# Kernel optimization log

Hardware: AMD Instinct MI355X
Metric: run time of the kernel (lower is better)

The kernel has to match this reference:

```python
import jax, jax.numpy as jnp
import numpy as np

N = 500_000      # total rows (e.g. video frames)
S = 10_000       # number of segments (shots)
D_IN = 128
D_OUT = 128


def setup_inputs() -> dict:
    key = jax.random.key(0)
    k1, k2, k3 = jax.random.split(key, 3)
    inp = jax.random.normal(k1, (N, D_IN), dtype=jnp.float32)
    # contiguous non-overlapping segments covering [0, N): graph[j] = (start_j, end_j) inclusive
    rng = np.random.default_rng(0)
    cuts = np.sort(rng.choice(np.arange(1, N), size=S - 1, replace=False))
    starts = np.concatenate([[0], cuts]).astype(np.int64)
    ends = np.concatenate([cuts - 1, [N - 1]]).astype(np.int64)
    graph = jnp.asarray(np.stack([starts, ends], axis=1))  # [S, 2]
    # nn.Linear params (kaiming-uniform-ish scale is irrelevant for correctness baseline)
    W = jax.random.normal(k2, (D_OUT, D_IN), dtype=jnp.float32) * (1.0 / np.sqrt(D_IN))
    b = jax.random.normal(k3, (D_OUT,), dtype=jnp.float32) * 0.01
    return {"input": inp, "graph": graph, "W": W, "b": b}


def reference(input, graph, W, b):
    # One big GEMM for the projection (instead of per-segment Linear calls) ...
    y = input @ W.T + b                              # [N, D_OUT]
    n = input.shape[0]
    s = graph.shape[0]
    starts = graph[:, 0]
    ends = graph[:, 1]
    rows = jnp.arange(n)
    # ... then a single irregular segment reduction over ragged boundaries.
    seg_id = jnp.clip(jnp.searchsorted(starts, rows, side="right") - 1, 0, s - 1)  # [N]
    valid = (rows >= starts[seg_id]) & (rows <= ends[seg_id])  # guards any uncovered rows
    y = jnp.where(valid[:, None], y, 0.0)
    return jax.ops.segment_sum(y, seg_id, num_segments=s)     # [S, D_OUT]
```

## Files before the change

### kernel.cpp

```cpp
#include <hip/hip_runtime.h>
#include <hip/hip_bf16.h>


#define D 128
#define D4 32

__device__ __forceinline__ void f4add(float4& a, const float4& v) {
  a.x += v.x; a.y += v.y; a.z += v.z; a.w += v.w;
}

__global__ __launch_bounds__(256) void seg_sum_kernel(
    const float* __restrict__ in, const int* __restrict__ graph,
    float* __restrict__ Xs, int N, int S) {
  int s   = blockIdx.x;
  int tid = threadIdx.x;
  int rg  = tid >> 5;
  int c4  = tid & 31;

  int rs  = graph[2 * s];
  int re  = graph[2 * s + 1];
  int nxt = (s + 1 < S) ? (graph[2 * s + 2] - 1) : (N - 1);
  re = min(re, min(nxt, N - 1));
  rs = max(rs, 0);
  int cnt = max(0, re - rs + 1);

  const float4* p = (const float4*)in + (size_t)rs * D4 + c4;
  float4 a0 = make_float4(0.f, 0.f, 0.f, 0.f);
  float4 a1 = make_float4(0.f, 0.f, 0.f, 0.f);

  int r = rg;
  for (; r + 8 < cnt; r += 16) {
    float4 v0 = p[r * D4];
    float4 v1 = p[(r + 8) * D4];
    f4add(a0, v0);
    f4add(a1, v1);
  }
  for (; r < cnt; r += 8) {
    float4 v0 = p[r * D4];
    f4add(a0, v0);
  }
  f4add(a0, a1);

  __shared__ float4 red[256];
  red[tid] = a0;
  __syncthreads();
  if (tid < 128) { f4add(red[tid], red[tid + 128]); }
  __syncthreads();
  if (tid < 64)  { f4add(red[tid], red[tid + 64]); }
  __syncthreads();
  if (tid < 32) {
    float4 r4 = red[tid];
    f4add(r4, red[tid + 32]);
    ((float4*)Xs)[s * D4 + tid] = r4;
  }
}

#define SEG_PB 16
#define OUT_PB 64
#define WT_STRIDE 65

__global__ __launch_bounds__(256) void seg_gemm_kernel(
    const float* __restrict__ Xs, const float* __restrict__ W,
    const float* __restrict__ b, const int* __restrict__ graph,
    float* __restrict__ out, int N, int S) {
  __shared__ float Wt[D * WT_STRIDE];
  __shared__ __align__(16) float XsL[SEG_PB * D];
  __shared__ float cntL[SEG_PB];

  int tid   = threadIdx.x;
  int s0    = blockIdx.x * SEG_PB;
  int oBase = blockIdx.y * OUT_PB;

  #pragma unroll
  for (int rnd = 0; rnd < 8; ++rnd) {
    int linear = rnd * 256 + tid;
    int op     = linear >> 5;
    int d4     = (linear & 31) << 2;
    float4 w = *(const float4*)(W + (oBase + op) * D + d4);
    Wt[(d4 + 0) * WT_STRIDE + op] = w.x;
    Wt[(d4 + 1) * WT_STRIDE + op] = w.y;
    Wt[(d4 + 2) * WT_STRIDE + op] = w.z;
    Wt[(d4 + 3) * WT_STRIDE + op] = w.w;
  }
  {
    const float4* src = (const float4*)(Xs + s0 * D);
    float4* dst = (float4*)XsL;
    dst[tid]       = src[tid];
    dst[tid + 256] = src[tid + 256];
  }
  if (tid < SEG_PB) {
    int s   = s0 + tid;
    int rs  = graph[2 * s];
    int re  = graph[2 * s + 1];
    int nxt = (s + 1 < S) ? (graph[2 * s + 2] - 1) : (N - 1);
    re = min(re, min(nxt, N - 1));
    rs = max(rs, 0);
    cntL[tid] = (float)max(0, re - rs + 1);
  }
  __syncthreads();

  int op = tid & 63;
  int g  = tid >> 6;
  float acc[4] = {0.f, 0.f, 0.f, 0.f};

  const float4* xs4 = (const float4*)XsL;
  #pragma unroll 8
  for (int d4 = 0; d4 < D4; ++d4) {
    float w0 = Wt[(4 * d4 + 0) * WT_STRIDE + op];
    float w1 = Wt[(4 * d4 + 1) * WT_STRIDE + op];
    float w2 = Wt[(4 * d4 + 2) * WT_STRIDE + op];
    float w3 = Wt[(4 * d4 + 3) * WT_STRIDE + op];
    #pragma unroll
    for (int j = 0; j < 4; ++j) {
      float4 x = xs4[(4 * j + g) * D4 + d4];
      acc[j] += x.x * w0 + x.y * w1 + x.z * w2 + x.w * w3;
    }
  }

  float bo = b[oBase + op];
  #pragma unroll
  for (int j = 0; j < 4; ++j) {
    int sl = 4 * j + g;
    out[(s0 + sl) * D + oBase + op] = acc[j] + cntL[sl] * bo;
  }
}

extern "C" void kernel_launch(void* const* d_in, const int* in_sizes, int n_in,
                              void* d_out, int out_size, void* d_ws, size_t ws_size,
                              hipStream_t stream) {
  const float* in    = (const float*)d_in[0];
  const int*   graph = (const int*)d_in[1];
  const float* W     = (const float*)d_in[2];
  const float* b     = (const float*)d_in[3];
  float* out = (float*)d_out;

  const int N = in_sizes[0] / D;
  const int S = in_sizes[1] / 2;

  float* Xs = (float*)d_ws;

  seg_sum_kernel<<<S, 256, 0, stream>>>(in, graph, Xs, N, S);

  dim3 grid2(S / SEG_PB, D / OUT_PB);
  seg_gemm_kernel<<<grid2, 256, 0, stream>>>(Xs, W, b, graph, out, N, S);
}
```

Baseline: 372.7 us.

## Assign one wavefront per segment with shuffle reduction instead of block-wide LDS

The segment-sum kernel now maps each segment to a single 64-lane wavefront (four segments per block) instead of a whole 256-thread block. Each wave reads two rows per step with four independent accumulators, and the two half-waves are combined with a cross-lane xor shuffle, removing the shared-memory reduction and its barriers. The aim is to cut per-segment synchronization overhead and idle threads on short segments. In exchange, each segment has less in-flight memory parallelism, and long segments may take longer per wave.

```diff
diff --git a/kernel.cpp b/kernel.cpp
--- a/kernel.cpp
+++ b/kernel.cpp
@@ -12,10 +12,11 @@
 __global__ __launch_bounds__(256) void seg_sum_kernel(
     const float* __restrict__ in, const int* __restrict__ graph,
     float* __restrict__ Xs, int N, int S) {
-  int s   = blockIdx.x;
-  int tid = threadIdx.x;
-  int rg  = tid >> 5;
-  int c4  = tid & 31;
+  int s = blockIdx.x * 4 + (threadIdx.x >> 6);
+  if (s >= S) return;
+  int lane = threadIdx.x & 63;
+  int rp   = lane >> 5;
+  int c4   = lane & 31;
 
   int rs  = graph[2 * s];
   int re  = graph[2 * s + 1];
@@ -27,31 +28,29 @@
   const float4* p = (const float4*)in + (size_t)rs * D4 + c4;
   float4 a0 = make_float4(0.f, 0.f, 0.f, 0.f);
   float4 a1 = make_float4(0.f, 0.f, 0.f, 0.f);
+  float4 a2 = make_float4(0.f, 0.f, 0.f, 0.f);
+  float4 a3 = make_float4(0.f, 0.f, 0.f, 0.f);
 
-  int r = rg;
-  for (; r + 8 < cnt; r += 16) {
-    float4 v0 = p[r * D4];
-    float4 v1 = p[(r + 8) * D4];
-    f4add(a0, v0);
-    f4add(a1, v1);
+  int r = rp;
+  for (; r + 6 < cnt; r += 8) {
+    float4 v0 = p[(size_t)(r    ) * D4];
+    float4 v1 = p[(size_t)(r + 2) * D4];
+    float4 v2 = p[(size_t)(r + 4) * D4];
+    float4 v3 = p[(size_t)(r + 6) * D4];
+    f4add(a0, v0); f4add(a1, v1); f4add(a2, v2); f4add(a3, v3);
   }
-  for (; r < cnt; r += 8) {
-    float4 v0 = p[r * D4];
-    f4add(a0, v0);
+  for (; r < cnt; r += 2) {
+    f4add(a0, p[(size_t)r * D4]);
   }
-  f4add(a0, a1);
+  f4add(a0, a1); f4add(a2, a3); f4add(a0, a2);
 
-  __shared__ float4 red[256];
-  red[tid] = a0;
-  __syncthreads();
-  if (tid < 128) { f4add(red[tid], red[tid + 128]); }
-  __syncthreads();
-  if (tid < 64)  { f4add(red[tid], red[tid + 64]); }
-  __syncthreads();
-  if (tid < 32) {
-    float4 r4 = red[tid];
-    f4add(r4, red[tid + 32]);
-    ((float4*)Xs)[s * D4 + tid] = r4;
+  a0.x += __shfl_xor(a0.x, 32);
+  a0.y += __shfl_xor(a0.y, 32);
+  a0.z += __shfl_xor(a0.z, 32);
+  a0.w += __shfl_xor(a0.w, 32);
+
+  if (rp == 0) {
+    ((float4*)Xs)[(size_t)s * D4 + c4] = a0;
   }
 }
 
@@ -139,7 +138,7 @@
 
   float* Xs = (float*)d_ws;
 
-  seg_sum_kernel<<<S, 256, 0, stream>>>(in, graph, Xs, N, S);
+  seg_sum_kernel<<<(S + 3) / 4, 256, 0, stream>>>(in, graph, Xs, N, S);
 
   dim3 grid2(S / SEG_PB, D / OUT_PB);
   seg_gemm_kernel<<<grid2, 256, 0, stream>>>(Xs, W, b, graph, out, N, S);
```

After: 386.5 us. +3.7%, slower.

## Split segment reduction into fixed row chunks with atomic merging of partial sums

Applied to the files above, without the earlier changes.

The segment-sum kernel now launches one block per fixed 128-row chunk instead of one block per segment. Each block binary-searches the graph for its first segment and reduces every segment overlapping the chunk. Segments that fit inside a chunk are stored directly, and segments crossing a chunk boundary are merged with float atomics into a buffer zeroed by a new kernel. The aim is to even out load across blocks despite ragged segment lengths. In exchange it adds a zero pass, a binary search per block, a block sync per segment, atomics, and unroll-by-4 accumulation.

```diff
diff --git a/kernel.cpp b/kernel.cpp
--- a/kernel.cpp
+++ b/kernel.cpp
@@ -4,54 +4,86 @@
 
 #define D 128
 #define D4 32
+#define CHUNK 128
 
 __device__ __forceinline__ void f4add(float4& a, const float4& v) {
   a.x += v.x; a.y += v.y; a.z += v.z; a.w += v.w;
 }
 
+__global__ __launch_bounds__(256) void zero_kernel(float4* __restrict__ Xs) {
+  Xs[blockIdx.x * 256 + threadIdx.x] = make_float4(0.f, 0.f, 0.f, 0.f);
+}
+
 __global__ __launch_bounds__(256) void seg_sum_kernel(
     const float* __restrict__ in, const int* __restrict__ graph,
     float* __restrict__ Xs, int N, int S) {
-  int s   = blockIdx.x;
+  __shared__ float4 red[256];
+
   int tid = threadIdx.x;
   int rg  = tid >> 5;
   int c4  = tid & 31;
 
-  int rs  = graph[2 * s];
-  int re  = graph[2 * s + 1];
-  int nxt = (s + 1 < S) ? (graph[2 * s + 2] - 1) : (N - 1);
-  re = min(re, min(nxt, N - 1));
-  rs = max(rs, 0);
-  int cnt = max(0, re - rs + 1);
+  int c0 = blockIdx.x * CHUNK;
+  int c1 = min(c0 + CHUNK, N);
 
-  const float4* p = (const float4*)in + (size_t)rs * D4 + c4;
-  float4 a0 = make_float4(0.f, 0.f, 0.f, 0.f);
-  float4 a1 = make_float4(0.f, 0.f, 0.f, 0.f);
+  int lo = 0, hi = S - 1;
+  while (lo < hi) {
+    int mid = (lo + hi + 1) >> 1;
+    if (graph[2 * mid] <= c0) lo = mid; else hi = mid - 1;
+  }
 
-  int r = rg;
-  for (; r + 8 < cnt; r += 16) {
-    float4 v0 = p[r * D4];
-    float4 v1 = p[(r + 8) * D4];
-    f4add(a0, v0);
-    f4add(a1, v1);
-  }
-  for (; r < cnt; r += 8) {
-    float4 v0 = p[r * D4];
-    f4add(a0, v0);
-  }
-  f4add(a0, a1);
+  for (int s = lo; s < S; ++s) {
+    int rs = graph[2 * s];
+    if (rs > c1 - 1) break;
+    int re  = graph[2 * s + 1];
+    int nxt = (s + 1 < S) ? (graph[2 * s + 2] - 1) : (N - 1);
+    re = min(re, min(nxt, N - 1));
+    rs = max(rs, 0);
 
-  __shared__ float4 red[256];
-  red[tid] = a0;
-  __syncthreads();
-  if (tid < 128) { f4add(red[tid], red[tid + 128]); }
-  __syncthreads();
-  if (tid < 64)  { f4add(red[tid], red[tid + 64]); }
-  __syncthreads();
-  if (tid < 32) {
-    float4 r4 = red[tid];
-    f4add(r4, red[tid + 32]);
-    ((float4*)Xs)[s * D4 + tid] = r4;
+    int rlo = max(rs, c0);
+    int rhi = min(re, c1 - 1);
+    if (rlo > rhi) continue;
+    int cnt = rhi - rlo + 1;
+
+    const float4* p = (const float4*)in + (size_t)rlo * D4 + c4;
+    float4 a0 = make_float4(0.f, 0.f, 0.f, 0.f);
+    float4 a1 = make_float4(0.f, 0.f, 0.f, 0.f);
+    float4 a2 = make_float4(0.f, 0.f, 0.f, 0.f);
+    float4 a3 = make_float4(0.f, 0.f, 0.f, 0.f);
+
+    int r = rg;
+    for (; r + 24 < cnt; r += 32) {
+      float4 v0 = p[(r     ) * D4];
+      float4 v1 = p[(r +  8) * D4];
+      float4 v2 = p[(r + 16) * D4];
+      float4 v3 = p[(r + 24) * D4];
+      f4add(a0, v0); f4add(a1, v1); f4add(a2, v2); f4add(a3, v3);
+    }
+    for (; r < cnt; r += 8) {
+      f4add(a0, p[r * D4]);
+    }
+    f4add(a0, a1); f4add(a2, a3); f4add(a0, a2);
+
+    red[tid] = a0;
+    __syncthreads();
+    if (tid < 128) { f4add(red[tid], red[tid + 128]); }
+    __syncthreads();
+    if (tid < 64)  { f4add(red[tid], red[tid + 64]); }
+    __syncthreads();
+    if (tid < 32) {
+      float4 r4 = red[tid];
+      f4add(r4, red[tid + 32]);
+      if (rs >= c0 && re <= c1 - 1) {
+        ((float4*)Xs)[(size_t)s * D4 + tid] = r4;
+      } else {
+        float* dst = Xs + (size_t)s * D + tid * 4;
+        atomicAdd(dst + 0, r4.x);
+        atomicAdd(dst + 1, r4.y);
+        atomicAdd(dst + 2, r4.z);
+        atomicAdd(dst + 3, r4.w);
+      }
+    }
+    __syncthreads();
   }
 }
 
@@ -139,7 +171,10 @@
 
   float* Xs = (float*)d_ws;
 
-  seg_sum_kernel<<<S, 256, 0, stream>>>(in, graph, Xs, N, S);
+  zero_kernel<<<(S * D4) / 256, 256, 0, stream>>>((float4*)Xs);
+
+  int nChunks = (N + CHUNK - 1) / CHUNK;
+  seg_sum_kernel<<<nChunks, 256, 0, stream>>>(in, graph, Xs, N, S);
 
   dim3 grid2(S / SEG_PB, D / OUT_PB);
   seg_gemm_kernel<<<grid2, 256, 0, stream>>>(Xs, W, b, graph, out, N, S);
```

After: 375.7 us. About the same (+0.8%).
